# Performance work log

Measured on AMD Instinct MI355X. Metric: run time of the kernel, lower is better.

## Reference

```python
import jax, jax.numpy as jnp
import numpy as np
import math

EMBED_DIM = 1024
N_HEADS = 16
QK_DIM = 64
V_DIM = 64
B, S = 4, 2048


def setup_inputs() -> dict:
    key = jax.random.key(0)
    ks = jax.random.split(key, 10)
    sc = lambda fan_in: 1.0 / math.sqrt(fan_in)
    X = jax.random.normal(ks[0], (B, S, EMBED_DIM), dtype=jnp.float32)
    mask = jax.random.randint(ks[1], (B, 1, S, S), 0, 2, dtype=jnp.int32)
    wQ = jax.random.uniform(ks[2], (EMBED_DIM, QK_DIM * N_HEADS), jnp.float32, -sc(EMBED_DIM), sc(EMBED_DIM))
    bQ = jnp.zeros((QK_DIM * N_HEADS,), jnp.float32)
    wK = jax.random.uniform(ks[3], (EMBED_DIM, QK_DIM * N_HEADS), jnp.float32, -sc(EMBED_DIM), sc(EMBED_DIM))
    bK = jnp.zeros((QK_DIM * N_HEADS,), jnp.float32)
    wV = jax.random.uniform(ks[4], (EMBED_DIM, V_DIM * N_HEADS), jnp.float32, -sc(EMBED_DIM), sc(EMBED_DIM))
    bV = jnp.zeros((V_DIM * N_HEADS,), jnp.float32)
    wO = jax.random.uniform(ks[5], (V_DIM * N_HEADS, EMBED_DIM), jnp.float32, -sc(V_DIM * N_HEADS), sc(V_DIM * N_HEADS))
    bO = jnp.zeros((EMBED_DIM,), jnp.float32)
    return {"X": X, "mask": mask, "wQ": wQ, "bQ": bQ, "wK": wK, "bK": bK,
            "wV": wV, "bV": bV, "wO": wO, "bO": bO}


def reference(X, mask, wQ, bQ, wK, bK, wV, bV, wO, bO):
    Bsz, Slen, _ = X.shape
    # projections -> [B, H, S, d]
    q = (X @ wQ + bQ).reshape(Bsz, Slen, N_HEADS, QK_DIM).transpose(0, 2, 1, 3)
    k = (X @ wK + bK).reshape(Bsz, Slen, N_HEADS, QK_DIM).transpose(0, 2, 1, 3)
    v = (X @ wV + bV).reshape(Bsz, Slen, N_HEADS, V_DIM).transpose(0, 2, 1, 3)
    # scores [B, H, S, S]
    scores = jnp.einsum("bhqd,bhkd->bhqk", q, k) / math.sqrt(QK_DIM)
    scores = jnp.where(mask == 0, jnp.float32(-1e9), scores)
    probs = jax.nn.softmax(scores, axis=-1)
    out = jnp.einsum("bhqk,bhkd->bhqd", probs, v)  # [B, H, S, v]
    out = out.transpose(0, 2, 1, 3).reshape(Bsz, Slen, N_HEADS * V_DIM)
    return out @ wO + bO
```

## Files before the change

kernel.cpp:

```cpp
#include <hip/hip_runtime.h>
#include <hip/hip_bf16.h>

#define EMB 1024
#define NH 16
#define DH 64
#define SEQ 2048

typedef __attribute__((ext_vector_type(8))) __bf16 bf16x8;
typedef __attribute__((ext_vector_type(4))) float f32x4;

__device__ __forceinline__ void g2l16(const void* g, void* l) {
  __builtin_amdgcn_global_load_lds(
      (const __attribute__((address_space(1))) void*)g,
      (__attribute__((address_space(3))) void*)l, 16, 0, 0);
}

__global__ void detect_k(const unsigned short* __restrict__ xs,
                         int* __restrict__ flag) {
  __shared__ int cnt;
  if (threadIdx.x == 0) cnt = 0;
  __syncthreads();
  int hits = 0;
  for (int i = threadIdx.x; i < 16384; i += 256) {
    unsigned e = (xs[i] >> 7) & 0xFFu;
    if (e >= 0xC0u) hits++;
  }
  atomicAdd(&cnt, hits);
  __syncthreads();
  if (threadIdx.x == 0) *flag = (cnt > 16) ? 1 : 0;
}

__global__ void conv_k(const void* __restrict__ src,
                       __hip_bfloat16* __restrict__ dst,
                       const int* __restrict__ flag, int n4) {
  int i = blockIdx.x * 256 + threadIdx.x;
  if (i >= n4) return;
  if (*flag) {
    float4 v = ((const float4*)src)[i];
    ushort4 o;
    __hip_bfloat16 t;
    t = __float2bfloat16(v.x); o.x = *(unsigned short*)&t;
    t = __float2bfloat16(v.y); o.y = *(unsigned short*)&t;
    t = __float2bfloat16(v.z); o.z = *(unsigned short*)&t;
    t = __float2bfloat16(v.w); o.w = *(unsigned short*)&t;
    ((ushort4*)dst)[i] = o;
  } else {
    ((ushort4*)dst)[i] = ((const ushort4*)src)[i];
  }
}

__global__ void convB_k(const void* s0, const void* s1, const void* s2,
                        const void* s3, __hip_bfloat16* __restrict__ dst,
                        const int* __restrict__ flag) {
  const void* srcs[4] = {s0, s1, s2, s3};
  const void* src = srcs[blockIdx.x];
  int i = threadIdx.x;
  __hip_bfloat16* d = dst + blockIdx.x * 1024;
  if (*flag) {
    float4 v = ((const float4*)src)[i];
    ushort4 o;
    __hip_bfloat16 t;
    t = __float2bfloat16(v.x); o.x = *(unsigned short*)&t;
    t = __float2bfloat16(v.y); o.y = *(unsigned short*)&t;
    t = __float2bfloat16(v.z); o.z = *(unsigned short*)&t;
    t = __float2bfloat16(v.w); o.w = *(unsigned short*)&t;
    ((ushort4*)d)[i] = o;
  } else {
    ((ushort4*)d)[i] = ((const ushort4*)src)[i];
  }
}

__global__ void transW4_k(const void* s0, const void* s1, const void* s2,
                          const void* s3, __hip_bfloat16* d0,
                          __hip_bfloat16* d1, __hip_bfloat16* d2,
                          __hip_bfloat16* d3, const int* __restrict__ flag) {
  __shared__ __hip_bfloat16 tile[32][33];
  const void* srcs[4] = {s0, s1, s2, s3};
  __hip_bfloat16* dsts[4] = {d0, d1, d2, d3};
  const void* src = srcs[blockIdx.z];
  __hip_bfloat16* dst = dsts[blockIdx.z];
  int f = *flag;
  int tx = threadIdx.x, ty = threadIdx.y;
  int x = blockIdx.x * 32 + tx;
  int y0 = blockIdx.y * 32;
  for (int i = 0; i < 32; i += 8) {
    int idx = (y0 + ty + i) * EMB + x;
    tile[ty + i][tx] = f ? __float2bfloat16(((const float*)src)[idx])
                         : ((const __hip_bfloat16*)src)[idx];
  }
  __syncthreads();
  int x2 = y0 + tx;
  int y2 = blockIdx.x * 32;
  for (int i = 0; i < 32; i += 8)
    dst[(size_t)(y2 + ty + i) * EMB + x2] = tile[tx][ty + i];
}

__global__ void maskpack_k(const int* __restrict__ mask,
                           unsigned int* __restrict__ bits) {
  int g = blockIdx.x * 256 + threadIdx.x;
  int lane = threadIdx.x & 63;
  unsigned long long bal = __ballot(mask[g] != 0);
  if ((lane & 31) == 0)
    bits[g >> 5] = (unsigned int)(bal >> (lane & 32));
}

__launch_bounds__(256)
__global__ void gemm_qkv(const __hip_bfloat16* __restrict__ A,
                         const __hip_bfloat16* __restrict__ Bt,
                         const __hip_bfloat16* __restrict__ bias,
                         __hip_bfloat16* __restrict__ CQ,
                         __hip_bfloat16* __restrict__ CK,
                         __hip_bfloat16* __restrict__ CV) {
  __shared__ __align__(16) __bf16 sA[128 * 32];
  __shared__ __align__(16) __bf16 sB[128 * 32];
  const __bf16* Ab = (const __bf16*)A;
  const __bf16* Bb = (const __bf16*)Bt;

  int tid = threadIdx.x;
  int w = tid >> 6, lane = tid & 63;
  int quad = lane >> 4, lcol = lane & 15;
  int m0 = blockIdx.x * 128, n0 = blockIdx.y * 128;
  int wm = (w >> 1) * 64, wn = (w & 1) * 64;
  int region = n0 >> 10;

  f32x4 z = {0.f, 0.f, 0.f, 0.f};
  f32x4 acc[4][4];
#pragma unroll
  for (int i = 0; i < 4; i++)
#pragma unroll
    for (int j = 0; j < 4; j++) acc[i][j] = z;

  int c = w * 64 + lane;
  int r = c >> 2, cc = c & 3;

  for (int k0 = 0; k0 < 1024; k0 += 32) {
    __syncthreads();
    g2l16(Ab + (size_t)(m0 + r) * 1024 + k0 + cc * 8, (char*)sA + w * 1024);
    g2l16(Ab + (size_t)(m0 + r + 64) * 1024 + k0 + cc * 8, (char*)sA + 4096 + w * 1024);
    g2l16(Bb + (size_t)(n0 + r) * 1024 + k0 + cc * 8, (char*)sB + w * 1024);
    g2l16(Bb + (size_t)(n0 + r + 64) * 1024 + k0 + cc * 8, (char*)sB + 4096 + w * 1024);
    __syncthreads();

    bf16x8 af[4], bfr[4];
#pragma unroll
    for (int i = 0; i < 4; i++)
      af[i] = *(const bf16x8*)(sA + (wm + i * 16 + lcol) * 32 + quad * 8);
#pragma unroll
    for (int j = 0; j < 4; j++)
      bfr[j] = *(const bf16x8*)(sB + (wn + j * 16 + lcol) * 32 + quad * 8);
#pragma unroll
    for (int i = 0; i < 4; i++)
#pragma unroll
      for (int j = 0; j < 4; j++)
        acc[i][j] = __builtin_amdgcn_mfma_f32_16x16x32_bf16(af[i], bfr[j], acc[i][j], 0, 0, 0);
  }

  float scale = (region == 0) ? 0.18033688011111204f : 1.0f;
#pragma unroll
  for (int j = 0; j < 4; j++) {
    int col = n0 + wn + j * 16 + lcol;
    float bv = __bfloat162float(bias[col]);
    int lc = col & 1023;
    int h = lc >> 6, dd = lc & 63;
#pragma unroll
    for (int i = 0; i < 4; i++) {
      int rbase = m0 + wm + i * 16 + quad * 4;
      int b = rbase >> 11, s = rbase & 2047;
      if (region == 1) {
#pragma unroll
        for (int rr = 0; rr < 4; rr++) {
          float v = acc[i][j][rr] + bv;
          CK[(((size_t)(b * NH + h)) * SEQ + s + rr) * DH + dd] = __float2bfloat16(v);
        }
      } else {
        union { unsigned long long u; __hip_bfloat16 bb[4]; } pk;
#pragma unroll
        for (int rr = 0; rr < 4; rr++)
          pk.bb[rr] = __float2bfloat16((acc[i][j][rr] + bv) * scale);
        __hip_bfloat16* dst = (region == 0) ? CQ : CV;
        *(unsigned long long*)(dst + (((size_t)(b * NH + h)) * DH + dd) * SEQ + s) = pk.u;
      }
    }
  }
}

__launch_bounds__(256)
__global__ void gemm_o(const __hip_bfloat16* __restrict__ A,
                       const __hip_bfloat16* __restrict__ Bt,
                       const __hip_bfloat16* __restrict__ bias,
                       void* __restrict__ Cv, const int* __restrict__ flag) {
  __shared__ __align__(16) __bf16 sA[128 * 32];
  __shared__ __align__(16) __bf16 sB[128 * 32];
  const __bf16* Ab = (const __bf16*)A;
  const __bf16* Bb = (const __bf16*)Bt;
  int f32out = *flag;

  int tid = threadIdx.x;
  int w = tid >> 6, lane = tid & 63;
  int quad = lane >> 4, lcol = lane & 15;
  int m0 = blockIdx.x * 128, n0 = blockIdx.y * 128;
  int wm = (w >> 1) * 64, wn = (w & 1) * 64;

  f32x4 z = {0.f, 0.f, 0.f, 0.f};
  f32x4 acc[4][4];
#pragma unroll
  for (int i = 0; i < 4; i++)
#pragma unroll
    for (int j = 0; j < 4; j++) acc[i][j] = z;

  int c = w * 64 + lane;
  int r = c >> 2, cc = c & 3;

  for (int k0 = 0; k0 < 1024; k0 += 32) {
    __syncthreads();
    g2l16(Ab + (size_t)(m0 + r) * 1024 + k0 + cc * 8, (char*)sA + w * 1024);
    g2l16(Ab + (size_t)(m0 + r + 64) * 1024 + k0 + cc * 8, (char*)sA + 4096 + w * 1024);
    g2l16(Bb + (size_t)(n0 + r) * 1024 + k0 + cc * 8, (char*)sB + w * 1024);
    g2l16(Bb + (size_t)(n0 + r + 64) * 1024 + k0 + cc * 8, (char*)sB + 4096 + w * 1024);
    __syncthreads();

    bf16x8 af[4], bfr[4];
#pragma unroll
    for (int i = 0; i < 4; i++)
      af[i] = *(const bf16x8*)(sA + (wm + i * 16 + lcol) * 32 + quad * 8);
#pragma unroll
    for (int j = 0; j < 4; j++)
      bfr[j] = *(const bf16x8*)(sB + (wn + j * 16 + lcol) * 32 + quad * 8);
#pragma unroll
    for (int i = 0; i < 4; i++)
#pragma unroll
      for (int j = 0; j < 4; j++)
        acc[i][j] = __builtin_amdgcn_mfma_f32_16x16x32_bf16(af[i], bfr[j], acc[i][j], 0, 0, 0);
  }

#pragma unroll
  for (int j = 0; j < 4; j++) {
    int col = n0 + wn + j * 16 + lcol;
    float bv = __bfloat162float(bias[col]);
#pragma unroll
    for (int i = 0; i < 4; i++) {
      int rbase = m0 + wm + i * 16 + quad * 4;
#pragma unroll
      for (int rr = 0; rr < 4; rr++) {
        int m = rbase + rr;
        float v = acc[i][j][rr] + bv;
        if (f32out)
          ((float*)Cv)[(size_t)m * EMB + col] = v;
        else
          ((__hip_bfloat16*)Cv)[(size_t)m * EMB + col] = __float2bfloat16(v);
      }
    }
  }
}

__launch_bounds__(256)
__global__ void attn_k(const __hip_bfloat16* __restrict__ Qt,
                       const __hip_bfloat16* __restrict__ Kp,
                       const __hip_bfloat16* __restrict__ Vp,
                       const unsigned int* __restrict__ mbits,
                       __hip_bfloat16* __restrict__ AO) {
  __shared__ __align__(16) __bf16 sK[64 * 64];
  __shared__ __align__(16) __bf16 sV[64 * 64];
  __shared__ __align__(16) __bf16 sP[4 * 16 * 72];
  __shared__ unsigned long long sLut[16];

  int tid = threadIdx.x;
  int w = tid >> 6, lane = tid & 63, quad = lane >> 4, lcol = lane & 15;
  int bid = blockIdx.y * 32 + blockIdx.x;
  int xcd = bid & 7, idx = bid >> 3;
  int bh = xcd * 8 + (idx >> 5);
  int qblk = idx & 31;
  int b = bh >> 4, h = bh & 15;

  if (tid < 16) {
    unsigned long long v = 0;
    if (tid & 1) v |= 0xFFFFull;
    if (tid & 2) v |= 0xFFFFull << 16;
    if (tid & 4) v |= 0xFFFFull << 32;
    if (tid & 8) v |= 0xFFFFull << 48;
    sLut[tid] = v;
  }

  const __bf16* Qb = (const __bf16*)Qt + (size_t)bh * DH * SEQ;
  const __bf16* Kb = (const __bf16*)Kp + (size_t)bh * SEQ * DH;
  const __bf16* Vb = (const __bf16*)Vp + (size_t)bh * DH * SEQ;
  int qw = qblk * 64 + w * 16;
  int q_mine = qw + lcol;

  union { bf16x8 v; __bf16 e[8]; } uq0, uq1;
#pragma unroll
  for (int j = 0; j < 8; j++) {
    uq0.e[j] = Qb[(size_t)(quad * 8 + j) * SEQ + q_mine];
    uq1.e[j] = Qb[(size_t)(32 + quad * 8 + j) * SEQ + q_mine];
  }
  bf16x8 bq0 = uq0.v, bq1 = uq1.v;

  __bf16 onev = (__bf16)1.0f;
  bf16x8 ones = {onev, onev, onev, onev, onev, onev, onev, onev};

  f32x4 z = {0.f, 0.f, 0.f, 0.f};
  f32x4 ot[4];
  f32x4 lacc = z;
#pragma unroll
  for (int j = 0; j < 4; j++) ot[j] = z;

  const unsigned long long* mrow =
      (const unsigned long long*)mbits + ((size_t)b * SEQ + q_mine) * (SEQ / 64);

  int kr = lane >> 3, pc = lane & 7;
  __bf16* pw = sP + w * (16 * 72);

  for (int kt = 0; kt < SEQ / 64; ++kt) {
    __syncthreads();
#pragma unroll
    for (int t2 = 0; t2 < 2; t2++) {
      int row = w * 16 + t2 * 8 + kr;
      g2l16(Kb + (size_t)(kt * 64 + row) * DH + (pc ^ kr) * 8,
            (char*)sK + (w * 16 + t2 * 8) * 128);
      g2l16(Vb + (size_t)row * SEQ + kt * 64 + (pc ^ kr) * 8,
            (char*)sV + (w * 16 + t2 * 8) * 128);
    }
    __syncthreads();

    f32x4 st[4];
    int swz = lcol & 7;
#pragma unroll
    for (int t = 0; t < 4; t++) {
      int rowK = t * 16 + lcol;
      bf16x8 a0 = *(const bf16x8*)(sK + rowK * 64 + (quad ^ swz) * 8);
      bf16x8 a1 = *(const bf16x8*)(sK + rowK * 64 + ((quad + 4) ^ swz) * 8);
      f32x4 sv = __builtin_amdgcn_mfma_f32_16x16x32_bf16(a0, bq0, z, 0, 0, 0);
      sv = __builtin_amdgcn_mfma_f32_16x16x32_bf16(a1, bq1, sv, 0, 0, 0);
      st[t] = sv;
    }

    unsigned long long mb64 = mrow[kt];
    unsigned int lo32 = (unsigned int)(mb64 >> (quad * 4));
    unsigned int hi32 = (unsigned int)(mb64 >> (quad * 4 + 32));
#pragma unroll
    for (int t = 0; t < 4; t++) {
      unsigned int sel = (t < 2) ? lo32 : hi32;
      unsigned int bits4 = (sel >> ((t & 1) * 16)) & 0xFu;
      union { unsigned long long u; __bf16 bb[4]; } pk;
#pragma unroll
      for (int r = 0; r < 4; r++)
        pk.bb[r] = (__bf16)__builtin_amdgcn_exp2f(fminf(st[t][r], 80.f));
      pk.u &= sLut[bits4];
      *(unsigned long long*)(pw + lcol * 72 + t * 16 + quad * 4) = pk.u;
    }

    bf16x8 bp0 = *(const bf16x8*)(pw + lcol * 72 + quad * 8);
    bf16x8 bp1 = *(const bf16x8*)(pw + lcol * 72 + 32 + quad * 8);
#pragma unroll
    for (int j = 0; j < 4; j++) {
      int rowV = j * 16 + lcol;
      bf16x8 av0 = *(const bf16x8*)(sV + rowV * 64 + (quad ^ swz) * 8);
      bf16x8 av1 = *(const bf16x8*)(sV + rowV * 64 + ((quad + 4) ^ swz) * 8);
      ot[j] = __builtin_amdgcn_mfma_f32_16x16x32_bf16(av0, bp0, ot[j], 0, 0, 0);
      ot[j] = __builtin_amdgcn_mfma_f32_16x16x32_bf16(av1, bp1, ot[j], 0, 0, 0);
    }
    lacc = __builtin_amdgcn_mfma_f32_16x16x32_bf16(ones, bp0, lacc, 0, 0, 0);
    lacc = __builtin_amdgcn_mfma_f32_16x16x32_bf16(ones, bp1, lacc, 0, 0, 0);
  }

  float linv = 1.0f / fmaxf(lacc[0], 1e-20f);
#pragma unroll
  for (int j = 0; j < 4; j++) {
    union { ushort4 u; __bf16 bb[4]; } pk;
#pragma unroll
    for (int r = 0; r < 4; r++) pk.bb[r] = (__bf16)(ot[j][r] * linv);
    *(ushort4*)((__bf16*)AO + ((size_t)b * SEQ + q_mine) * EMB + h * 64 +
                j * 16 + quad * 4) = pk.u;
  }
}

extern "C" void kernel_launch(void* const* d_in, const int* in_sizes, int n_in,
                              void* d_out, int out_size, void* d_ws, size_t ws_size,
                              hipStream_t stream) {
  const int* mask = (const int*)d_in[1];

  char* ws = (char*)d_ws;
  int* flag             = (int*)ws;
  __hip_bfloat16* biasc = (__hip_bfloat16*)(ws + (64ull << 10));
  __hip_bfloat16* WQt   = (__hip_bfloat16*)(ws + (1ull << 20));
  __hip_bfloat16* WKt   = (__hip_bfloat16*)(ws + (3ull << 20));
  __hip_bfloat16* WVt   = (__hip_bfloat16*)(ws + (5ull << 20));
  __hip_bfloat16* WOt   = (__hip_bfloat16*)(ws + (7ull << 20));
  unsigned int* mbits   = (unsigned int*)(ws + (9ull << 20));
  __hip_bfloat16* Xc    = (__hip_bfloat16*)(ws + (12ull << 20));
  __hip_bfloat16* Qw    = (__hip_bfloat16*)(ws + (28ull << 20));
  __hip_bfloat16* Kw    = (__hip_bfloat16*)(ws + (44ull << 20));
  __hip_bfloat16* Vtw   = (__hip_bfloat16*)(ws + (60ull << 20));
  __hip_bfloat16* AO    = (__hip_bfloat16*)(ws + (76ull << 20));

  detect_k<<<1, 256, 0, stream>>>((const unsigned short*)d_in[0], flag);

  conv_k<<<8192, 256, 0, stream>>>(d_in[0], Xc, flag, 2097152);
  convB_k<<<4, 256, 0, stream>>>(d_in[3], d_in[5], d_in[7], d_in[9], biasc, flag);

  dim3 tb(32, 8);
  transW4_k<<<dim3(32, 32, 4), tb, 0, stream>>>(d_in[2], d_in[4], d_in[6],
                                                d_in[8], WQt, WKt, WVt, WOt, flag);
  maskpack_k<<<65536, 256, 0, stream>>>(mask, mbits);

  gemm_qkv<<<dim3(64, 24), 256, 0, stream>>>(Xc, WQt, biasc, Qw, Kw, Vtw);
  attn_k<<<dim3(32, 64), 256, 0, stream>>>(Qw, Kw, Vtw, mbits, AO);
  gemm_o<<<dim3(64, 8), 256, 0, stream>>>(AO, WOt, biasc + 3072, d_out, flag);
}
```

Before: 427.4 us.

## Double-buffer K/V tiles and process two query tiles per wave in attention

```diff
diff --git a/kernel.cpp b/kernel.cpp
--- a/kernel.cpp
+++ b/kernel.cpp
@@ -259,17 +259,17 @@
                        const __hip_bfloat16* __restrict__ Vp,
                        const unsigned int* __restrict__ mbits,
                        __hip_bfloat16* __restrict__ AO) {
-  __shared__ __align__(16) __bf16 sK[64 * 64];
-  __shared__ __align__(16) __bf16 sV[64 * 64];
-  __shared__ __align__(16) __bf16 sP[4 * 16 * 72];
+  __shared__ __align__(16) __bf16 sK[2 * 64 * 64];
+  __shared__ __align__(16) __bf16 sV[2 * 64 * 64];
+  __shared__ __align__(16) __bf16 sP[4 * 2 * 16 * 72];
   __shared__ unsigned long long sLut[16];
 
   int tid = threadIdx.x;
   int w = tid >> 6, lane = tid & 63, quad = lane >> 4, lcol = lane & 15;
-  int bid = blockIdx.y * 32 + blockIdx.x;
+  int bid = blockIdx.x;
   int xcd = bid & 7, idx = bid >> 3;
-  int bh = xcd * 8 + (idx >> 5);
-  int qblk = idx & 31;
+  int bh = xcd * 8 + (idx >> 4);
+  int qblk = idx & 15;
   int b = bh >> 4, h = bh & 15;
 
   if (tid < 16) {
@@ -284,57 +284,51 @@
   const __bf16* Qb = (const __bf16*)Qt + (size_t)bh * DH * SEQ;
   const __bf16* Kb = (const __bf16*)Kp + (size_t)bh * SEQ * DH;
   const __bf16* Vb = (const __bf16*)Vp + (size_t)bh * DH * SEQ;
-  int qw = qblk * 64 + w * 16;
-  int q_mine = qw + lcol;
-
-  union { bf16x8 v; __bf16 e[8]; } uq0, uq1;
+  int qbase = qblk * 128 + w * 32;
+  int q0 = qbase + lcol;
+  int q1 = qbase + 16 + lcol;
+
+  union { bf16x8 v; __bf16 e[8]; } u0a, u0b, u1a, u1b;
 #pragma unroll
   for (int j = 0; j < 8; j++) {
-    uq0.e[j] = Qb[(size_t)(quad * 8 + j) * SEQ + q_mine];
-    uq1.e[j] = Qb[(size_t)(32 + quad * 8 + j) * SEQ + q_mine];
-  }
-  bf16x8 bq0 = uq0.v, bq1 = uq1.v;
+    u0a.e[j] = Qb[(size_t)(quad * 8 + j) * SEQ + q0];
+    u0b.e[j] = Qb[(size_t)(32 + quad * 8 + j) * SEQ + q0];
+    u1a.e[j] = Qb[(size_t)(quad * 8 + j) * SEQ + q1];
+    u1b.e[j] = Qb[(size_t)(32 + quad * 8 + j) * SEQ + q1];
+  }
+  bf16x8 bq0a = u0a.v, bq0b = u0b.v, bq1a = u1a.v, bq1b = u1b.v;
 
   __bf16 onev = (__bf16)1.0f;
   bf16x8 ones = {onev, onev, onev, onev, onev, onev, onev, onev};
 
   f32x4 z = {0.f, 0.f, 0.f, 0.f};
-  f32x4 ot[4];
-  f32x4 lacc = z;
-#pragma unroll
-  for (int j = 0; j < 4; j++) ot[j] = z;
-
-  const unsigned long long* mrow =
-      (const unsigned long long*)mbits + ((size_t)b * SEQ + q_mine) * (SEQ / 64);
+  f32x4 ot0[4], ot1[4];
+  f32x4 lacc0 = z, lacc1 = z;
+#pragma unroll
+  for (int j = 0; j < 4; j++) { ot0[j] = z; ot1[j] = z; }
+
+  const unsigned long long* mrow0 =
+      (const unsigned long long*)mbits + ((size_t)b * SEQ + q0) * (SEQ / 64);
+  const unsigned long long* mrow1 =
+      (const unsigned long long*)mbits + ((size_t)b * SEQ + q1) * (SEQ / 64);
 
   int kr = lane >> 3, pc = lane & 7;
-  __bf16* pw = sP + w * (16 * 72);
-
-  for (int kt = 0; kt < SEQ / 64; ++kt) {
-    __syncthreads();
+  __bf16* pw0 = sP + w * (2 * 16 * 72);
+  __bf16* pw1 = pw0 + 16 * 72;
+  int swz = lcol & 7;
+
+  auto STAGE = [&](int buf, int kt) {
 #pragma unroll
     for (int t2 = 0; t2 < 2; t2++) {
       int row = w * 16 + t2 * 8 + kr;
       g2l16(Kb + (size_t)(kt * 64 + row) * DH + (pc ^ kr) * 8,
-            (char*)sK + (w * 16 + t2 * 8) * 128);
+            (char*)sK + buf * 8192 + (w * 16 + t2 * 8) * 128);
       g2l16(Vb + (size_t)row * SEQ + kt * 64 + (pc ^ kr) * 8,
-            (char*)sV + (w * 16 + t2 * 8) * 128);
-    }
-    __syncthreads();
-
-    f32x4 st[4];
-    int swz = lcol & 7;
-#pragma unroll
-    for (int t = 0; t < 4; t++) {
-      int rowK = t * 16 + lcol;
-      bf16x8 a0 = *(const bf16x8*)(sK + rowK * 64 + (quad ^ swz) * 8);
-      bf16x8 a1 = *(const bf16x8*)(sK + rowK * 64 + ((quad + 4) ^ swz) * 8);
-      f32x4 sv = __builtin_amdgcn_mfma_f32_16x16x32_bf16(a0, bq0, z, 0, 0, 0);
-      sv = __builtin_amdgcn_mfma_f32_16x16x32_bf16(a1, bq1, sv, 0, 0, 0);
-      st[t] = sv;
-    }
-
-    unsigned long long mb64 = mrow[kt];
+            (char*)sV + buf * 8192 + (w * 16 + t2 * 8) * 128);
+    }
+  };
+
+  auto PACK = [&](f32x4 (&st)[4], unsigned long long mb64, __bf16* pw) {
     unsigned int lo32 = (unsigned int)(mb64 >> (quad * 4));
     unsigned int hi32 = (unsigned int)(mb64 >> (quad * 4 + 32));
 #pragma unroll
@@ -348,29 +342,71 @@
       pk.u &= sLut[bits4];
       *(unsigned long long*)(pw + lcol * 72 + t * 16 + quad * 4) = pk.u;
     }
-
-    bf16x8 bp0 = *(const bf16x8*)(pw + lcol * 72 + quad * 8);
-    bf16x8 bp1 = *(const bf16x8*)(pw + lcol * 72 + 32 + quad * 8);
+  };
+
+  STAGE(0, 0);
+  __syncthreads();
+
+  for (int kt = 0; kt < SEQ / 64; ++kt) {
+    int cur = kt & 1;
+    const __bf16* sKc = sK + cur * 4096;
+    const __bf16* sVc = sV + cur * 4096;
+    if (kt + 1 < SEQ / 64) STAGE(cur ^ 1, kt + 1);
+
+    f32x4 st0[4], st1[4];
+#pragma unroll
+    for (int t = 0; t < 4; t++) {
+      int rowK = t * 16 + lcol;
+      bf16x8 a0 = *(const bf16x8*)(sKc + rowK * 64 + (quad ^ swz) * 8);
+      bf16x8 a1 = *(const bf16x8*)(sKc + rowK * 64 + ((quad + 4) ^ swz) * 8);
+      f32x4 s0 = __builtin_amdgcn_mfma_f32_16x16x32_bf16(a0, bq0a, z, 0, 0, 0);
+      s0 = __builtin_amdgcn_mfma_f32_16x16x32_bf16(a1, bq0b, s0, 0, 0, 0);
+      f32x4 s1 = __builtin_amdgcn_mfma_f32_16x16x32_bf16(a0, bq1a, z, 0, 0, 0);
+      s1 = __builtin_amdgcn_mfma_f32_16x16x32_bf16(a1, bq1b, s1, 0, 0, 0);
+      st0[t] = s0;
+      st1[t] = s1;
+    }
+
+    PACK(st0, mrow0[kt], pw0);
+    PACK(st1, mrow1[kt], pw1);
+
+    bf16x8 bp00 = *(const bf16x8*)(pw0 + lcol * 72 + quad * 8);
+    bf16x8 bp01 = *(const bf16x8*)(pw0 + lcol * 72 + 32 + quad * 8);
+    bf16x8 bp10 = *(const bf16x8*)(pw1 + lcol * 72 + quad * 8);
+    bf16x8 bp11 = *(const bf16x8*)(pw1 + lcol * 72 + 32 + quad * 8);
+
 #pragma unroll
     for (int j = 0; j < 4; j++) {
       int rowV = j * 16 + lcol;
-      bf16x8 av0 = *(const bf16x8*)(sV + rowV * 64 + (quad ^ swz) * 8);
-      bf16x8 av1 = *(const bf16x8*)(sV + rowV * 64 + ((quad + 4) ^ swz) * 8);
-      ot[j] = __builtin_amdgcn_mfma_f32_16x16x32_bf16(av0, bp0, ot[j], 0, 0, 0);
-      ot[j] = __builtin_amdgcn_mfma_f32_16x16x32_bf16(av1, bp1, ot[j], 0, 0, 0);
-    }
-    lacc = __builtin_amdgcn_mfma_f32_16x16x32_bf16(ones, bp0, lacc, 0, 0, 0);
-    lacc = __builtin_amdgcn_mfma_f32_16x16x32_bf16(ones, bp1, lacc, 0, 0, 0);
-  }
-
-  float linv = 1.0f / fmaxf(lacc[0], 1e-20f);
+      bf16x8 av0 = *(const bf16x8*)(sVc + rowV * 64 + (quad ^ swz) * 8);
+      bf16x8 av1 = *(const bf16x8*)(sVc + rowV * 64 + ((quad + 4) ^ swz) * 8);
+      ot0[j] = __builtin_amdgcn_mfma_f32_16x16x32_bf16(av0, bp00, ot0[j], 0, 0, 0);
+      ot0[j] = __builtin_amdgcn_mfma_f32_16x16x32_bf16(av1, bp01, ot0[j], 0, 0, 0);
+      ot1[j] = __builtin_amdgcn_mfma_f32_16x16x32_bf16(av0, bp10, ot1[j], 0, 0, 0);
+      ot1[j] = __builtin_amdgcn_mfma_f32_16x16x32_bf16(av1, bp11, ot1[j], 0, 0, 0);
+    }
+    lacc0 = __builtin_amdgcn_mfma_f32_16x16x32_bf16(ones, bp00, lacc0, 0, 0, 0);
+    lacc0 = __builtin_amdgcn_mfma_f32_16x16x32_bf16(ones, bp01, lacc0, 0, 0, 0);
+    lacc1 = __builtin_amdgcn_mfma_f32_16x16x32_bf16(ones, bp10, lacc1, 0, 0, 0);
+    lacc1 = __builtin_amdgcn_mfma_f32_16x16x32_bf16(ones, bp11, lacc1, 0, 0, 0);
+
+    __syncthreads();
+  }
+
+  float linv0 = 1.0f / fmaxf(lacc0[0], 1e-20f);
+  float linv1 = 1.0f / fmaxf(lacc1[0], 1e-20f);
 #pragma unroll
   for (int j = 0; j < 4; j++) {
-    union { ushort4 u; __bf16 bb[4]; } pk;
-#pragma unroll
-    for (int r = 0; r < 4; r++) pk.bb[r] = (__bf16)(ot[j][r] * linv);
-    *(ushort4*)((__bf16*)AO + ((size_t)b * SEQ + q_mine) * EMB + h * 64 +
-                j * 16 + quad * 4) = pk.u;
+    union { ushort4 u; __bf16 bb[4]; } pk0, pk1;
+#pragma unroll
+    for (int r = 0; r < 4; r++) {
+      pk0.bb[r] = (__bf16)(ot0[j][r] * linv0);
+      pk1.bb[r] = (__bf16)(ot1[j][r] * linv1);
+    }
+    *(ushort4*)((__bf16*)AO + ((size_t)b * SEQ + q0) * EMB + h * 64 +
+                j * 16 + quad * 4) = pk0.u;
+    *(ushort4*)((__bf16*)AO + ((size_t)b * SEQ + q1) * EMB + h * 64 +
+                j * 16 + quad * 4) = pk1.u;
   }
 }
 
@@ -404,6 +440,6 @@
   maskpack_k<<<65536, 256, 0, stream>>>(mask, mbits);
 
   gemm_qkv<<<dim3(64, 24), 256, 0, stream>>>(Xc, WQt, biasc, Qw, Kw, Vtw);
-  attn_k<<<dim3(32, 64), 256, 0, stream>>>(Qw, Kw, Vtw, mbits, AO);
+  attn_k<<<dim3(1024), 256, 0, stream>>>(Qw, Kw, Vtw, mbits, AO);
   gemm_o<<<dim3(64, 8), 256, 0, stream>>>(AO, WOt, biasc + 3072, d_out, flag);
 }
```

After: 435.0 us. Within noise of the previous version (+1.8%).

## Double-buffer K/V tiles in attention and prefetch mask bits

Applied to the files above, without the earlier changes.

```diff
diff --git a/kernel.cpp b/kernel.cpp
--- a/kernel.cpp
+++ b/kernel.cpp
@@ -259,8 +259,8 @@
                        const __hip_bfloat16* __restrict__ Vp,
                        const unsigned int* __restrict__ mbits,
                        __hip_bfloat16* __restrict__ AO) {
-  __shared__ __align__(16) __bf16 sK[64 * 64];
-  __shared__ __align__(16) __bf16 sV[64 * 64];
+  __shared__ __align__(16) __bf16 sK[2 * 64 * 64];
+  __shared__ __align__(16) __bf16 sV[2 * 64 * 64];
   __shared__ __align__(16) __bf16 sP[4 * 16 * 72];
   __shared__ unsigned long long sLut[16];
 
@@ -309,34 +309,45 @@
 
   int kr = lane >> 3, pc = lane & 7;
   __bf16* pw = sP + w * (16 * 72);
-
-  for (int kt = 0; kt < SEQ / 64; ++kt) {
-    __syncthreads();
+  int swz = lcol & 7;
+
+  auto STAGE = [&](int buf, int kt) {
 #pragma unroll
     for (int t2 = 0; t2 < 2; t2++) {
       int row = w * 16 + t2 * 8 + kr;
       g2l16(Kb + (size_t)(kt * 64 + row) * DH + (pc ^ kr) * 8,
-            (char*)sK + (w * 16 + t2 * 8) * 128);
+            (char*)sK + buf * 8192 + (w * 16 + t2 * 8) * 128);
       g2l16(Vb + (size_t)row * SEQ + kt * 64 + (pc ^ kr) * 8,
-            (char*)sV + (w * 16 + t2 * 8) * 128);
-    }
-    __syncthreads();
+            (char*)sV + buf * 8192 + (w * 16 + t2 * 8) * 128);
+    }
+  };
+
+  STAGE(0, 0);
+  unsigned long long mb = mrow[0];
+  __syncthreads();
+
+  for (int kt = 0; kt < SEQ / 64; ++kt) {
+    int cur = kt & 1;
+    const __bf16* sKc = sK + cur * 4096;
+    const __bf16* sVc = sV + cur * 4096;
+    if (kt < SEQ / 64 - 1) STAGE(cur ^ 1, kt + 1);
+    unsigned long long mb_next = mrow[(kt + 1) & (SEQ / 64 - 1)];
 
     f32x4 st[4];
-    int swz = lcol & 7;
+    __builtin_amdgcn_s_setprio(1);
 #pragma unroll
     for (int t = 0; t < 4; t++) {
       int rowK = t * 16 + lcol;
-      bf16x8 a0 = *(const bf16x8*)(sK + rowK * 64 + (quad ^ swz) * 8);
-      bf16x8 a1 = *(const bf16x8*)(sK + rowK * 64 + ((quad + 4) ^ swz) * 8);
+      bf16x8 a0 = *(const bf16x8*)(sKc + rowK * 64 + (quad ^ swz) * 8);
+      bf16x8 a1 = *(const bf16x8*)(sKc + rowK * 64 + ((quad + 4) ^ swz) * 8);
       f32x4 sv = __builtin_amdgcn_mfma_f32_16x16x32_bf16(a0, bq0, z, 0, 0, 0);
       sv = __builtin_amdgcn_mfma_f32_16x16x32_bf16(a1, bq1, sv, 0, 0, 0);
       st[t] = sv;
     }
-
-    unsigned long long mb64 = mrow[kt];
-    unsigned int lo32 = (unsigned int)(mb64 >> (quad * 4));
-    unsigned int hi32 = (unsigned int)(mb64 >> (quad * 4 + 32));
+    __builtin_amdgcn_s_setprio(0);
+
+    unsigned int lo32 = (unsigned int)(mb >> (quad * 4));
+    unsigned int hi32 = (unsigned int)(mb >> (quad * 4 + 32));
 #pragma unroll
     for (int t = 0; t < 4; t++) {
       unsigned int sel = (t < 2) ? lo32 : hi32;
@@ -344,23 +355,28 @@
       union { unsigned long long u; __bf16 bb[4]; } pk;
 #pragma unroll
       for (int r = 0; r < 4; r++)
-        pk.bb[r] = (__bf16)__builtin_amdgcn_exp2f(fminf(st[t][r], 80.f));
+        pk.bb[r] = (__bf16)__builtin_amdgcn_exp2f(st[t][r]);
       pk.u &= sLut[bits4];
       *(unsigned long long*)(pw + lcol * 72 + t * 16 + quad * 4) = pk.u;
     }
 
     bf16x8 bp0 = *(const bf16x8*)(pw + lcol * 72 + quad * 8);
     bf16x8 bp1 = *(const bf16x8*)(pw + lcol * 72 + 32 + quad * 8);
+    __builtin_amdgcn_s_setprio(1);
 #pragma unroll
     for (int j = 0; j < 4; j++) {
       int rowV = j * 16 + lcol;
-      bf16x8 av0 = *(const bf16x8*)(sV + rowV * 64 + (quad ^ swz) * 8);
-      bf16x8 av1 = *(const bf16x8*)(sV + rowV * 64 + ((quad + 4) ^ swz) * 8);
+      bf16x8 av0 = *(const bf16x8*)(sVc + rowV * 64 + (quad ^ swz) * 8);
+      bf16x8 av1 = *(const bf16x8*)(sVc + rowV * 64 + ((quad + 4) ^ swz) * 8);
       ot[j] = __builtin_amdgcn_mfma_f32_16x16x32_bf16(av0, bp0, ot[j], 0, 0, 0);
       ot[j] = __builtin_amdgcn_mfma_f32_16x16x32_bf16(av1, bp1, ot[j], 0, 0, 0);
     }
     lacc = __builtin_amdgcn_mfma_f32_16x16x32_bf16(ones, bp0, lacc, 0, 0, 0);
     lacc = __builtin_amdgcn_mfma_f32_16x16x32_bf16(ones, bp1, lacc, 0, 0, 0);
+    __builtin_amdgcn_s_setprio(0);
+
+    mb = mb_next;
+    __syncthreads();
   }
 
   float linv = 1.0f / fmaxf(lacc[0], 1e-20f);
```

Result: no change. 428.6 us (+0.3%).
